# Kernel tuning notes

Measured on AMD Instinct MI355X. Metric: run time of the kernel, lower is better.

The kernel has to match this reference:

```python
import jax, jax.numpy as jnp
import numpy as np

B, C, H, W = 32, 17, 256, 256


def setup_inputs() -> dict:
    key = jax.random.key(0)
    k1, k2 = jax.random.split(key)
    inp = jax.random.normal(k1, (B, C, H, W), dtype=jnp.float32)
    tgt = jax.random.normal(k2, (B, C, H, W), dtype=jnp.float32)
    masks = jnp.zeros((B, C, H, W), dtype=bool)  # unused by forward
    hull = jnp.zeros((B, 1, H, W), dtype=bool)   # unused by forward
    return {"input": inp, "target": tgt, "masks": masks, "hull": hull}


def reference(input, target, masks, hull):
    # m1: per-(batch, channel) mask of positive target pixels
    m1 = target > 0.0                                  # [B,C,H,W] bool
    # m2: per-batch OR over channels, broadcast back to every channel.
    # (replaces the original O(B*C) Python double loop)
    m2 = jnp.any(m1, axis=1, keepdims=True)            # [B,1,H,W] bool
    diff = jnp.abs(input - target)                     # [B,C,H,W]
    f32 = jnp.float32
    # masked means without data-dependent shapes: sum(mask*diff)/sum(mask)
    mean1 = jnp.sum(jnp.where(m1, diff, f32(0))) / jnp.sum(m1).astype(f32)
    cnt2 = jnp.sum(m2).astype(f32) * f32(diff.shape[1])  # broadcast over C channels
    mean2 = jnp.sum(jnp.where(m2, diff, f32(0))) / cnt2
    return (mean1 + mean2) / f32(2)
```

## Files before the change

kernel.cpp:

```cpp
#include <hip/hip_runtime.h>


#define QPB      16384
#define N_CH     17
#define N_BATCH  32
#define N_QUADS  (N_BATCH * QPB)
#define N_BLOCKS 2048

struct Slot {
    float s1;
    float s2;
    unsigned int c1;
    unsigned int c2;
};

__global__ __launch_bounds__(256, 2) void heatloss_stage1(
    const float* __restrict__ inp, const float* __restrict__ tgt,
    Slot* __restrict__ slots) {

    const int q = blockIdx.x * 256 + threadIdx.x;
    const int b = q >> 14;
    const int r = q & (QPB - 1);

    const float4* __restrict__ tp = (const float4*)tgt + (size_t)b * (N_CH * QPB) + r;
    const float4* __restrict__ xp = (const float4*)inp + (size_t)b * (N_CH * QPB) + r;

    float4 t[N_CH];
    float4 x[N_CH];
    #pragma unroll
    for (int c = 0; c < N_CH; ++c) t[c] = tp[(size_t)c * QPB];
    #pragma unroll
    for (int c = 0; c < N_CH; ++c) x[c] = xp[(size_t)c * QPB];

    float s1 = 0.0f;
    unsigned int c1 = 0u;
    float sa0 = 0.f, sa1 = 0.f, sa2 = 0.f, sa3 = 0.f;
    bool a0 = false, a1 = false, a2 = false, a3 = false;

    #pragma unroll
    for (int c = 0; c < N_CH; ++c) {
        float d0 = fabsf(x[c].x - t[c].x);
        float d1 = fabsf(x[c].y - t[c].y);
        float d2 = fabsf(x[c].z - t[c].z);
        float d3 = fabsf(x[c].w - t[c].w);
        bool p0 = t[c].x > 0.f, p1 = t[c].y > 0.f, p2 = t[c].z > 0.f, p3 = t[c].w > 0.f;
        sa0 += d0; sa1 += d1; sa2 += d2; sa3 += d3;
        s1 += p0 ? d0 : 0.f;  c1 += p0 ? 1u : 0u;  a0 = a0 || p0;
        s1 += p1 ? d1 : 0.f;  c1 += p1 ? 1u : 0u;  a1 = a1 || p1;
        s1 += p2 ? d2 : 0.f;  c1 += p2 ? 1u : 0u;  a2 = a2 || p2;
        s1 += p3 ? d3 : 0.f;  c1 += p3 ? 1u : 0u;  a3 = a3 || p3;
    }
    float s2 = (a0 ? sa0 : 0.f) + (a1 ? sa1 : 0.f) + (a2 ? sa2 : 0.f) + (a3 ? sa3 : 0.f);
    unsigned int c2 = (a0 ? 1u : 0u) + (a1 ? 1u : 0u) + (a2 ? 1u : 0u) + (a3 ? 1u : 0u);

    #pragma unroll
    for (int off = 32; off > 0; off >>= 1) {
        s1 += __shfl_down(s1, off);
        s2 += __shfl_down(s2, off);
        c1 += __shfl_down(c1, off);
        c2 += __shfl_down(c2, off);
    }

    __shared__ float ls1[4], ls2[4];
    __shared__ unsigned int lc1[4], lc2[4];
    const int wave = threadIdx.x >> 6;
    const int lane = threadIdx.x & 63;
    if (lane == 0) {
        ls1[wave] = s1; ls2[wave] = s2;
        lc1[wave] = c1; lc2[wave] = c2;
    }
    __syncthreads();
    if (threadIdx.x == 0) {
        Slot sl;
        sl.s1 = ls1[0] + ls1[1] + ls1[2] + ls1[3];
        sl.s2 = ls2[0] + ls2[1] + ls2[2] + ls2[3];
        sl.c1 = lc1[0] + lc1[1] + lc1[2] + lc1[3];
        sl.c2 = lc2[0] + lc2[1] + lc2[2] + lc2[3];
        slots[blockIdx.x] = sl;
    }
}

__global__ __launch_bounds__(256) void heatloss_stage2(
    const Slot* __restrict__ slots, float* __restrict__ out) {

    float s1 = 0.f, s2 = 0.f;
    unsigned int c1 = 0u, c2 = 0u;
    for (int i = threadIdx.x; i < N_BLOCKS; i += 256) {
        Slot sl = slots[i];
        s1 += sl.s1; s2 += sl.s2; c1 += sl.c1; c2 += sl.c2;
    }
    #pragma unroll
    for (int off = 32; off > 0; off >>= 1) {
        s1 += __shfl_down(s1, off);
        s2 += __shfl_down(s2, off);
        c1 += __shfl_down(c1, off);
        c2 += __shfl_down(c2, off);
    }
    __shared__ float ls1[4], ls2[4];
    __shared__ unsigned int lc1[4], lc2[4];
    const int wave = threadIdx.x >> 6;
    const int lane = threadIdx.x & 63;
    if (lane == 0) {
        ls1[wave] = s1; ls2[wave] = s2;
        lc1[wave] = c1; lc2[wave] = c2;
    }
    __syncthreads();
    if (threadIdx.x == 0) {
        float S1 = ls1[0] + ls1[1] + ls1[2] + ls1[3];
        float S2 = ls2[0] + ls2[1] + ls2[2] + ls2[3];
        float C1 = (float)(lc1[0] + lc1[1] + lc1[2] + lc1[3]);
        float C2 = (float)(lc2[0] + lc2[1] + lc2[2] + lc2[3]);
        float mean1 = S1 / C1;
        float mean2 = S2 / (C2 * (float)N_CH);
        out[0] = 0.5f * (mean1 + mean2);
    }
}

extern "C" void kernel_launch(void* const* d_in, const int* in_sizes, int n_in,
                              void* d_out, int out_size, void* d_ws, size_t ws_size,
                              hipStream_t stream) {
    const float* inp = (const float*)d_in[0];
    const float* tgt = (const float*)d_in[1];
    float* out = (float*)d_out;
    Slot* slots = (Slot*)d_ws;

    heatloss_stage1<<<N_BLOCKS, 256, 0, stream>>>(inp, tgt, slots);
    heatloss_stage2<<<1, 256, 0, stream>>>(slots, out);
}
```

Before: 350.0 us.

## Replace full-register channel preload with rolling prefetch and raise occupancy

Result: no change. 346.9 us (-0.9%).

```diff
diff --git a/kernel.cpp b/kernel.cpp
--- a/kernel.cpp
+++ b/kernel.cpp
@@ -6,6 +6,7 @@
 #define N_BATCH  32
 #define N_QUADS  (N_BATCH * QPB)
 #define N_BLOCKS 2048
+#define PF       3
 
 struct Slot {
     float s1;
@@ -14,23 +15,24 @@
     unsigned int c2;
 };
 
-__global__ __launch_bounds__(256, 2) void heatloss_stage1(
+__global__ __launch_bounds__(256, 8) void heatloss_stage1(
     const float* __restrict__ inp, const float* __restrict__ tgt,
     Slot* __restrict__ slots) {
 
-    const int q = blockIdx.x * 256 + threadIdx.x;
+    const int blk = (blockIdx.x & 7) * (N_BLOCKS / 8) + (blockIdx.x >> 3);
+    const int q = blk * 256 + threadIdx.x;
     const int b = q >> 14;
     const int r = q & (QPB - 1);
 
     const float4* __restrict__ tp = (const float4*)tgt + (size_t)b * (N_CH * QPB) + r;
     const float4* __restrict__ xp = (const float4*)inp + (size_t)b * (N_CH * QPB) + r;
 
-    float4 t[N_CH];
-    float4 x[N_CH];
+    float4 tb[PF], xb[PF];
     #pragma unroll
-    for (int c = 0; c < N_CH; ++c) t[c] = tp[(size_t)c * QPB];
-    #pragma unroll
-    for (int c = 0; c < N_CH; ++c) x[c] = xp[(size_t)c * QPB];
+    for (int i = 0; i < PF; ++i) {
+        tb[i] = tp[(size_t)i * QPB];
+        xb[i] = xp[(size_t)i * QPB];
+    }
 
     float s1 = 0.0f;
     unsigned int c1 = 0u;
@@ -39,11 +41,18 @@
 
     #pragma unroll
     for (int c = 0; c < N_CH; ++c) {
-        float d0 = fabsf(x[c].x - t[c].x);
-        float d1 = fabsf(x[c].y - t[c].y);
-        float d2 = fabsf(x[c].z - t[c].z);
-        float d3 = fabsf(x[c].w - t[c].w);
-        bool p0 = t[c].x > 0.f, p1 = t[c].y > 0.f, p2 = t[c].z > 0.f, p3 = t[c].w > 0.f;
+        const int slot = c % PF;
+        float4 t = tb[slot];
+        float4 x = xb[slot];
+        if (c + PF < N_CH) {
+            tb[slot] = tp[(size_t)(c + PF) * QPB];
+            xb[slot] = xp[(size_t)(c + PF) * QPB];
+        }
+        float d0 = fabsf(x.x - t.x);
+        float d1 = fabsf(x.y - t.y);
+        float d2 = fabsf(x.z - t.z);
+        float d3 = fabsf(x.w - t.w);
+        bool p0 = t.x > 0.f, p1 = t.y > 0.f, p2 = t.z > 0.f, p3 = t.w > 0.f;
         sa0 += d0; sa1 += d1; sa2 += d2; sa3 += d3;
         s1 += p0 ? d0 : 0.f;  c1 += p0 ? 1u : 0u;  a0 = a0 || p0;
         s1 += p1 ? d1 : 0.f;  c1 += p1 ? 1u : 0u;  a1 = a1 || p1;
```
